# Performance work log

Hardware: AMD Instinct MI355X
Metric: run time of the kernel (lower is better)

The kernel has to match this reference:

```python
import jax, jax.numpy as jnp
import numpy as np

NB = 10          # number_of_basis (hardcoded in module)
MAX_RADIUS = 3.5
DIM_SH = 16      # spherical harmonics l = 0..3 -> (3+1)^2 components


def spherical_harmonics_l3(vec):
    # real spherical harmonics l=0..3 of the normalized vector,
    # 'component' normalization (each component has unit variance on S^2)
    r = jnp.sqrt(jnp.sum(vec * vec, -1, keepdims=True))
    u = vec / jnp.maximum(r, 1e-9)
    x, y, z = u[..., 0], u[..., 1], u[..., 2]
    s3, s5, s15 = jnp.sqrt(3.0), jnp.sqrt(5.0), jnp.sqrt(15.0)
    c358 = jnp.sqrt(35.0 / 8.0); c218 = jnp.sqrt(21.0 / 8.0)
    sh = [jnp.ones_like(x),
          s3 * x, s3 * y, s3 * z,
          s15 * x * y, s15 * y * z, (s5 / 2) * (3 * z * z - 1),
          s15 * x * z, (s15 / 2) * (x * x - y * y),
          c358 * y * (3 * x * x - y * y), jnp.sqrt(105.0) * x * y * z,
          c218 * y * (5 * z * z - 1), (jnp.sqrt(7.0) / 2) * z * (5 * z * z - 3),
          c218 * x * (5 * z * z - 1), (jnp.sqrt(105.0) / 2) * z * (x * x - y * y),
          c358 * x * (x * x - 3 * y * y)]
    return jnp.stack(sh, -1)  # [E, 16]


def soft_one_hot(r):
    # e3nn soft_one_hot_linspace, basis='smooth_finite', cutoff=True
    values = jnp.linspace(0.0, MAX_RADIUS, NB + 2)[1:-1]
    step = MAX_RADIUS / (NB + 1)
    u = (r[:, None] - values) / step
    mask = jnp.abs(u) < 1.0
    us = jnp.where(mask, u, 0.0)
    y = jnp.where(mask, jnp.exp(-1.0 / (1.0 - us * us)), 0.0)
    return 1.14136 * jnp.exp(2.0) * y * jnp.sqrt(float(NB))  # * number_of_basis**0.5


def soft_unit_step(t):
    ts = jnp.where(t > 0, t, 1.0)
    return jnp.where(t > 0, jnp.exp(-1.0 / ts), 0.0)


def fcnet(e, W1, W2):
    # e3nn FullyConnectedNet([10, 16, weight_numel], act=silu): bias-free,
    # fan-in normalized linear layers
    h = jax.nn.silu(e @ W1 / jnp.sqrt(float(e.shape[-1])))
    return h @ W2 / jnp.sqrt(float(W1.shape[-1]))


def setup_inputs() -> dict:
    key = jax.random.key(0)
    ks = jax.random.split(key, 9)
    N, E, C, DK = 20000, 50000, 16, 8
    pos = jax.random.uniform(ks[0], (N, 3), jnp.float32) * 2.0  # box so most edges < max_radius
    x = jax.random.normal(ks[1], (N, C), jnp.float32)
    Wq = jax.random.normal(ks[2], (C, DK), jnp.float32)
    Wk1 = jax.random.normal(ks[3], (NB, 16), jnp.float32)
    Wk2 = jax.random.normal(ks[4], (16, C * DIM_SH * DK), jnp.float32)
    Wv1 = jax.random.normal(ks[5], (NB, 16), jnp.float32)
    Wv2 = jax.random.normal(ks[6], (16, C * DIM_SH * DK), jnp.float32)
    edge_src = jax.random.randint(ks[7], (E,), 0, N, jnp.int32)
    edge_dst = jax.random.randint(ks[8], (E,), 0, N, jnp.int32)
    return {"pos": pos, "x": x, "Wq": Wq, "Wk1": Wk1, "Wk2": Wk2,
            "Wv1": Wv1, "Wv2": Wv2, "edge_src": edge_src, "edge_dst": edge_dst}


def reference(pos, x, Wq, Wk1, Wk2, Wv1, Wv2, edge_src, edge_dst):
    N, C = x.shape
    E = edge_src.shape[0]
    DK = Wq.shape[1]
    edge_vec = pos[edge_src] - pos[edge_dst]                    # [E, 3]
    r = jnp.sqrt(jnp.sum(edge_vec * edge_vec, -1) + 1e-18)      # [E]
    emb = soft_one_hot(r)                                       # [E, 10]
    cutoff = soft_unit_step(10.0 * (1.0 - r / MAX_RADIUS))      # [E]
    sh = spherical_harmonics_l3(edge_vec)                       # [E, 16]
    # per-edge weight-conditioned tensor products (shared_weights=False)
    wk = fcnet(emb, Wk1, Wk2).reshape(E, C, DIM_SH, DK)
    wv = fcnet(emb, Wv1, Wv2).reshape(E, C, DIM_SH, DK)
    xs = x[edge_src]                                            # gather [E, C]
    norm = jnp.sqrt(float(C * DIM_SH))
    k = jnp.einsum('ec,ej,ecjo->eo', xs, sh, wk) / norm         # [E, DK]
    v = jnp.einsum('ec,ej,ecjo->eo', xs, sh, wv) / norm         # [E, DK]
    q = x @ Wq                                                  # [N, DK]
    logits = jnp.sum(q[edge_dst] * k, -1) / jnp.sqrt(float(DK)) # [E]
    expv = cutoff * jnp.exp(logits)
    z = jax.ops.segment_sum(expv, edge_dst, num_segments=N)     # segment-softmax denom
    z = jnp.where(z == 0.0, 1.0, z)
    alpha = expv / z[edge_dst]
    w = jnp.sqrt(jax.nn.relu(alpha))
    out = jax.ops.segment_sum(w[:, None] * v, edge_dst, num_segments=N)  # [N, DK]
    return out
```

## Files before the change

### kernel.cpp

```cpp
#include <hip/hip_runtime.h>
#include <hip/hip_bf16.h>

#define NBASIS 10
#define CDIM 16
#define DKDIM 8
#define JDIM 16

typedef _Float16 half8 __attribute__((ext_vector_type(8)));
typedef float floatx4 __attribute__((ext_vector_type(4)));

__device__ __forceinline__ float ldf(const void* p, int i, int f32) {
    if (f32) return ((const float*)p)[i];
    return __bfloat162float(((const __hip_bfloat16*)p)[i]);
}

__device__ __forceinline__ int detect_f32(const void* x) {
    unsigned short b = ((const unsigned short*)x)[threadIdx.x & 63];
    float v = __uint_as_float(((unsigned int)b) << 16);
    bool bad = !(fabsf(v) < 1000.0f) || (v != 0.0f && fabsf(v) < 1e-15f);
    unsigned long long m = __ballot(bad);
    return (__popcll(m) >= 8) ? 1 : 0;
}

__device__ __forceinline__ const float* uniform_ptr(const float* p) {
    uint64_t v = (uint64_t)p;
    uint32_t lo = __builtin_amdgcn_readfirstlane((uint32_t)v);
    uint32_t hi = __builtin_amdgcn_readfirstlane((uint32_t)(v >> 32));
    return (const float*)(((uint64_t)hi << 32) | lo);
}

__global__ __launch_bounds__(256) void prep_kernel(
    const void* __restrict__ x, const void* __restrict__ Wq,
    const void* __restrict__ Wk1, const void* __restrict__ Wk2,
    const void* __restrict__ Wv1, const void* __restrict__ Wv2,
    float* __restrict__ w1k, float* __restrict__ w1v,
    float* __restrict__ qbuf, _Float16* __restrict__ Bpk,
    int* __restrict__ head, int N)
{
    const int f32 = detect_f32(x);
    int i = blockIdx.x * 256 + threadIdx.x;
    if (i < 160) { w1k[i] = ldf(Wk1, i, f32); w1v[i] = ldf(Wv1, i, f32); }
    if (i < 65536) {
        int j = i & 7, lane = (i >> 3) & 63, ks = (i >> 9) & 7, nt = i >> 12;
        int kk = ks * 32 + (lane >> 4) * 8 + j;
        int nn = nt * 16 + (lane & 15);
        int c = kk >> 4, jj = kk & 15;
        int net = nn >> 7, m = (nn >> 3) & 15, o = nn & 7;
        float v = ldf(net ? Wv2 : Wk2, m * 2048 + c * 128 + jj * 8 + o, f32);
        Bpk[i] = (_Float16)v;
    }
    if (i < N) head[i] = -1;
    if (i < N * 8) {
        int n = i >> 3, o = i & 7;
        float acc = 0.0f;
        #pragma unroll
        for (int c = 0; c < CDIM; ++c)
            acc = fmaf(ldf(x, n * CDIM + c, f32), ldf(Wq, c * DKDIM + o, f32), acc);
        qbuf[i] = acc;
    }
}

__global__ __launch_bounds__(256) void edge_kernel(
    const void* __restrict__ pos, const void* __restrict__ x,
    const int* __restrict__ esrc, const int* __restrict__ edst,
    const float* __restrict__ w1k, const float* __restrict__ w1v,
    const float* __restrict__ qbuf, const _Float16* __restrict__ Bpk,
    int* __restrict__ head, int* __restrict__ next,
    float* __restrict__ evb, _Float16* __restrict__ vbuf, int E)
{
    __shared__ union {
        struct { float xs[64][17]; float sh[64][17]; } g;
        _Float16 A[16384];
        struct { float pk[2][64][9]; float pv[2][64][9]; } p;
    } u;
    __shared__ _Float16 hm_lds[64][34];
    __shared__ float cut_lds[64];
    __shared__ int   d_lds[64];

    const int f32  = detect_f32(x);
    const int tid  = threadIdx.x;
    const int lane = tid & 63;
    const int w    = tid >> 6;
    const int q    = lane >> 4;
    const int e0   = blockIdx.x * 64;
    const int e_g  = e0 + lane;
    const int eidx = (e_g < E) ? e_g : (E - 1);
    const int s = esrc[eidx], d = edst[eidx];

    int prev = -1;
    if (w == 0 && e_g < E) prev = atomicExch(&head[d], e_g);

    float vx = ldf(pos, s * 3 + 0, f32) - ldf(pos, d * 3 + 0, f32);
    float vy = ldf(pos, s * 3 + 1, f32) - ldf(pos, d * 3 + 1, f32);
    float vz = ldf(pos, s * 3 + 2, f32) - ldf(pos, d * 3 + 2, f32);
    float r2 = vx * vx + vy * vy + vz * vz;
    float r  = sqrtf(r2 + 1e-18f);

    if (w == 0) {
        float rsh = sqrtf(r2);
        float inv = 1.0f / fmaxf(rsh, 1e-9f);
        float ux = vx * inv, uy = vy * inv, uz = vz * inv;
        const float s3   = 1.7320508075688772f;
        const float s5   = 2.23606797749979f;
        const float s15  = 3.872983346207417f;
        const float c358 = 2.091650066335189f;
        const float c218 = 1.6201851746019651f;
        const float s105 = 10.246950765959598f;
        const float s7h  = 1.3228756555322954f;
        float xx = ux * ux, yy = uy * uy, zz = uz * uz;
        float sh[16];
        sh[0] = 1.0f;
        sh[1] = s3 * ux; sh[2] = s3 * uy; sh[3] = s3 * uz;
        sh[4] = s15 * ux * uy;
        sh[5] = s15 * uy * uz;
        sh[6] = 0.5f * s5 * (3.0f * zz - 1.0f);
        sh[7] = s15 * ux * uz;
        sh[8] = 0.5f * s15 * (xx - yy);
        sh[9] = c358 * uy * (3.0f * xx - yy);
        sh[10] = s105 * ux * uy * uz;
        sh[11] = c218 * uy * (5.0f * zz - 1.0f);
        sh[12] = s7h * uz * (5.0f * zz - 3.0f);
        sh[13] = c218 * ux * (5.0f * zz - 1.0f);
        sh[14] = 0.5f * s105 * uz * (xx - yy);
        sh[15] = c358 * ux * (xx - 3.0f * yy);
        #pragma unroll
        for (int j = 0; j < 16; ++j) u.g.sh[lane][j] = sh[j];
        float tcut = 10.0f * (1.0f - r * (1.0f / 3.5f));
        cut_lds[lane] = (tcut > 0.0f) ? expf(-1.0f / tcut) : 0.0f;
        d_lds[lane] = d;
    } else if (w == 1) {
        #pragma unroll
        for (int c = 0; c < CDIM; ++c)
            u.g.xs[lane][c] = ldf(x, s * CDIM + c, f32);
    } else {
        const float* w1 = uniform_ptr((w == 2) ? w1k : w1v);
        const int off = (w == 2) ? 0 : 16;
        float emb[NBASIS];
        const float step = 3.5f / 11.0f;
        const float istep = 11.0f / 3.5f;
        const float coef = (float)(1.14136 * 7.38905609893065 * 3.1622776601683795);
        #pragma unroll
        for (int i = 0; i < NBASIS; ++i) {
            float uu = (r - step * (float)(i + 1)) * istep; uu *= uu;
            emb[i] = (uu < 1.0f) ? coef * expf(-1.0f / (1.0f - uu)) : 0.0f;
        }
        const float inv_s10 = 0.31622776601683794f;
        #pragma unroll
        for (int m = 0; m < 16; ++m) {
            float pre = 0.0f;
            #pragma unroll
            for (int nb = 0; nb < NBASIS; ++nb)
                pre = fmaf(emb[nb], w1[nb * 16 + m], pre);
            pre *= inv_s10;
            hm_lds[lane][off + m] = (_Float16)(pre / (1.0f + expf(-pre)));
        }
    }
    __syncthreads();

    half8 af[8];
    {
        const int erow = w * 16 + (lane & 15);
        const int coff = q >> 1, jj0 = (q & 1) * 8;
        #pragma unroll
        for (int ks = 0; ks < 8; ++ks) {
            float xsv = u.g.xs[erow][ks * 2 + coff];
            half8 a;
            #pragma unroll
            for (int j = 0; j < 8; ++j)
                a[j] = (_Float16)(xsv * u.g.sh[erow][jj0 + j]);
            af[ks] = a;
        }
    }
    __syncthreads();
    {
        half8* Af = (half8*)u.A;
        #pragma unroll
        for (int ks = 0; ks < 8; ++ks)
            Af[(w * 8 + ks) * 64 + lane] = af[ks];
    }
    if (w == 0 && e_g < E) next[e_g] = prev;
    __syncthreads();

    float part[16];
    #pragma unroll
    for (int i = 0; i < 16; ++i) part[i] = 0.0f;
    const int b3   = (lane >> 3) & 1;
    const int moff = (w >> 1) * 16;
    const half8* Af = (const half8*)u.A;
    const half8* Bf = (const half8*)Bpk;

    #pragma unroll
    for (int rp = 0; rp < 2; ++rp) {
        half8 a0[8], a1[8];
        #pragma unroll
        for (int ks = 0; ks < 8; ++ks) {
            a0[ks] = Af[((2 * rp)     * 8 + ks) * 64 + lane];
            a1[ks] = Af[((2 * rp + 1) * 8 + ks) * 64 + lane];
        }
        floatx4 acc0[4], acc1[4];
        #pragma unroll
        for (int l = 0; l < 4; ++l) {
            acc0[l] = (floatx4){0.f, 0.f, 0.f, 0.f};
            acc1[l] = (floatx4){0.f, 0.f, 0.f, 0.f};
        }
        #pragma unroll
        for (int l = 0; l < 4; ++l) {
            const int nt = 4 * w + l;
            #pragma unroll
            for (int ks = 0; ks < 8; ++ks) {
                half8 b = Bf[(nt * 8 + ks) * 64 + lane];
                acc0[l] = __builtin_amdgcn_mfma_f32_16x16x32_f16(a0[ks], b, acc0[l], 0, 0, 0);
                acc1[l] = __builtin_amdgcn_mfma_f32_16x16x32_f16(a1[ks], b, acc1[l], 0, 0, 0);
            }
        }
        #pragma unroll
        for (int l = 0; l < 4; ++l) {
            const int m = ((4 * w + l) * 2 + b3) & 15;
            #pragma unroll
            for (int rr = 0; rr < 4; ++rr) {
                const int er = q * 4 + rr;
                part[(2 * rp) * 4 + rr] +=
                    (float)hm_lds[(2 * rp) * 16 + er][moff + m] * acc0[l][rr];
                part[(2 * rp + 1) * 4 + rr] +=
                    (float)hm_lds[(2 * rp + 1) * 16 + er][moff + m] * acc1[l][rr];
            }
        }
    }
    #pragma unroll
    for (int i = 0; i < 16; ++i) part[i] += __shfl_xor(part[i], 8, 64);

    __syncthreads();
    if (b3 == 0) {
        const int o = lane & 7;
        #pragma unroll
        for (int i = 0; i < 16; ++i) {
            const int e = (i >> 2) * 16 + q * 4 + (i & 3);
            if (w < 2) u.p.pk[w][e][o] = part[i];
            else       u.p.pv[w - 2][e][o] = part[i];
        }
    }
    __syncthreads();

    if (tid < 64) {
        const int dd = d_lds[tid];
        float logit = 0.0f;
        #pragma unroll
        for (int o = 0; o < 8; ++o) {
            float kv = u.p.pk[0][tid][o] + u.p.pk[1][tid][o];
            logit = fmaf(qbuf[(size_t)dd * 8 + o], kv, logit);
        }
        logit *= (1.0f / 64.0f) * 0.35355339059327373f;
        if (e0 + tid < E)
            evb[e0 + tid] = cut_lds[tid] * expf(logit);
    }

    {
        const int el = tid & 63, op = tid >> 6;
        if (e0 + el < E) {
            float v0 = u.p.pv[0][el][2 * op]     + u.p.pv[1][el][2 * op];
            float v1 = u.p.pv[0][el][2 * op + 1] + u.p.pv[1][el][2 * op + 1];
            vbuf[(size_t)(e0 + el) * 8 + 2 * op]     = (_Float16)(v0 * (1.0f / 64.0f));
            vbuf[(size_t)(e0 + el) * 8 + 2 * op + 1] = (_Float16)(v1 * (1.0f / 64.0f));
        }
    }
}

__global__ __launch_bounds__(256) void node_kernel(
    const float* __restrict__ evb, const _Float16* __restrict__ vbuf,
    const int* __restrict__ head, const int* __restrict__ next,
    void* __restrict__ out, const void* __restrict__ x, int n8)
{
    const int f32 = detect_f32(x);
    int i = blockIdx.x * 256 + threadIdx.x;
    if (i >= n8) return;
    const int n = i >> 3, o = i & 7;
    float z = 0.0f;
    for (int e = head[n]; e >= 0; e = next[e]) z += evb[e];
    z = (z == 0.0f) ? 1.0f : z;
    const float invz = 1.0f / z;
    float acc = 0.0f;
    for (int e = head[n]; e >= 0; e = next[e])
        acc += sqrtf(evb[e] * invz) * (float)vbuf[(size_t)e * 8 + o];
    if (f32) ((float*)out)[i] = acc;
    else ((__hip_bfloat16*)out)[i] = __float2bfloat16(acc);
}

extern "C" void kernel_launch(void* const* d_in, const int* in_sizes, int n_in,
                              void* d_out, int out_size, void* d_ws, size_t ws_size,
                              hipStream_t stream)
{
    const void* pos = d_in[0];
    const void* x   = d_in[1];
    const void* Wq  = d_in[2];
    const void* Wk1 = d_in[3];
    const void* Wk2 = d_in[4];
    const void* Wv1 = d_in[5];
    const void* Wv2 = d_in[6];
    const int* esrc = (const int*)d_in[7];
    const int* edst = (const int*)d_in[8];
    const int N = in_sizes[1] / CDIM;
    const int E = in_sizes[7];

    _Float16* Bpk = (_Float16*)d_ws;
    float* w1k  = (float*)(Bpk + 65536);
    float* w1v  = w1k + 160;
    float* qbuf = w1v + 160;
    float* evb  = qbuf + (size_t)N * 8;
    _Float16* vbuf = (_Float16*)(evb + E);
    int*   head = (int*)(vbuf + (size_t)E * 8);
    int*   next = head + N;

    int prep_threads = N * 8 > 65536 ? N * 8 : 65536;
    int prep_blocks = (prep_threads + 255) / 256;
    prep_kernel<<<prep_blocks, 256, 0, stream>>>(x, Wq, Wk1, Wk2, Wv1, Wv2,
                                                 w1k, w1v, qbuf, Bpk, head, N);

    int edge_blocks = (E + 63) / 64;
    edge_kernel<<<edge_blocks, 256, 0, stream>>>(pos, x, esrc, edst,
                                                 w1k, w1v, qbuf, Bpk,
                                                 head, next, evb, vbuf, E);

    node_kernel<<<(N * 8 + 255) / 256, 256, 0, stream>>>(
        evb, vbuf, head, next, d_out, x, N * 8);
}
```

Baseline: 101.4 us.

## Compute query projection per edge, pack vbuf stores, single-pass node reduction

Removes the per-node q = x@Wq precompute from the prep kernel. Each edge now computes q for its destination inside the edge kernel from x[dst] and Wq, with the logit scale folded in, and stages it in LDS. The v stores are packed into 32-bit writes. The node kernel walks the linked list once, accumulating both z and sqrt(ev)*v, then divides by sqrt(z) at the end instead of making two passes. The trade is redundant q computation per edge (16x8 FMAs plus an extra x gather) against fewer prep threads, no qbuf traffic, and half the list traversals.

```diff
diff --git a/kernel.cpp b/kernel.cpp
--- a/kernel.cpp
+++ b/kernel.cpp
@@ -30,12 +30,11 @@
 }
 
 __global__ __launch_bounds__(256) void prep_kernel(
-    const void* __restrict__ x, const void* __restrict__ Wq,
+    const void* __restrict__ x,
     const void* __restrict__ Wk1, const void* __restrict__ Wk2,
     const void* __restrict__ Wv1, const void* __restrict__ Wv2,
     float* __restrict__ w1k, float* __restrict__ w1v,
-    float* __restrict__ qbuf, _Float16* __restrict__ Bpk,
-    int* __restrict__ head, int N)
+    _Float16* __restrict__ Bpk, int* __restrict__ head, int N)
 {
     const int f32 = detect_f32(x);
     int i = blockIdx.x * 256 + threadIdx.x;
@@ -50,21 +49,14 @@
         Bpk[i] = (_Float16)v;
     }
     if (i < N) head[i] = -1;
-    if (i < N * 8) {
-        int n = i >> 3, o = i & 7;
-        float acc = 0.0f;
-        #pragma unroll
-        for (int c = 0; c < CDIM; ++c)
-            acc = fmaf(ldf(x, n * CDIM + c, f32), ldf(Wq, c * DKDIM + o, f32), acc);
-        qbuf[i] = acc;
-    }
 }
 
 __global__ __launch_bounds__(256) void edge_kernel(
     const void* __restrict__ pos, const void* __restrict__ x,
+    const void* __restrict__ Wq,
     const int* __restrict__ esrc, const int* __restrict__ edst,
     const float* __restrict__ w1k, const float* __restrict__ w1v,
-    const float* __restrict__ qbuf, const _Float16* __restrict__ Bpk,
+    const _Float16* __restrict__ Bpk,
     int* __restrict__ head, int* __restrict__ next,
     float* __restrict__ evb, _Float16* __restrict__ vbuf, int E)
 {
@@ -75,7 +67,7 @@
     } u;
     __shared__ _Float16 hm_lds[64][34];
     __shared__ float cut_lds[64];
-    __shared__ int   d_lds[64];
+    __shared__ float q_lds[64][9];
 
     const int f32  = detect_f32(x);
     const int tid  = threadIdx.x;
@@ -127,11 +119,22 @@
         for (int j = 0; j < 16; ++j) u.g.sh[lane][j] = sh[j];
         float tcut = 10.0f * (1.0f - r * (1.0f / 3.5f));
         cut_lds[lane] = (tcut > 0.0f) ? expf(-1.0f / tcut) : 0.0f;
-        d_lds[lane] = d;
     } else if (w == 1) {
-        #pragma unroll
-        for (int c = 0; c < CDIM; ++c)
+        float xd[CDIM];
+        #pragma unroll
+        for (int c = 0; c < CDIM; ++c) {
             u.g.xs[lane][c] = ldf(x, s * CDIM + c, f32);
+            xd[c] = ldf(x, d * CDIM + c, f32);
+        }
+        const float qscale = (1.0f / 64.0f) * 0.35355339059327373f;
+        #pragma unroll
+        for (int o = 0; o < 8; ++o) {
+            float acc = 0.0f;
+            #pragma unroll
+            for (int c = 0; c < CDIM; ++c)
+                acc = fmaf(xd[c], ldf(Wq, c * DKDIM + o, f32), acc);
+            q_lds[lane][o] = acc * qscale;
+        }
     } else {
         const float* w1 = uniform_ptr((w == 2) ? w1k : w1v);
         const int off = (w == 2) ? 0 : 16;
@@ -242,14 +245,12 @@
     __syncthreads();
 
     if (tid < 64) {
-        const int dd = d_lds[tid];
         float logit = 0.0f;
         #pragma unroll
         for (int o = 0; o < 8; ++o) {
             float kv = u.p.pk[0][tid][o] + u.p.pk[1][tid][o];
-            logit = fmaf(qbuf[(size_t)dd * 8 + o], kv, logit);
-        }
-        logit *= (1.0f / 64.0f) * 0.35355339059327373f;
+            logit = fmaf(q_lds[tid][o], kv, logit);
+        }
         if (e0 + tid < E)
             evb[e0 + tid] = cut_lds[tid] * expf(logit);
     }
@@ -259,8 +260,10 @@
         if (e0 + el < E) {
             float v0 = u.p.pv[0][el][2 * op]     + u.p.pv[1][el][2 * op];
             float v1 = u.p.pv[0][el][2 * op + 1] + u.p.pv[1][el][2 * op + 1];
-            vbuf[(size_t)(e0 + el) * 8 + 2 * op]     = (_Float16)(v0 * (1.0f / 64.0f));
-            vbuf[(size_t)(e0 + el) * 8 + 2 * op + 1] = (_Float16)(v1 * (1.0f / 64.0f));
+            union { _Float16 h[2]; unsigned int b; } pk2;
+            pk2.h[0] = (_Float16)(v0 * (1.0f / 64.0f));
+            pk2.h[1] = (_Float16)(v1 * (1.0f / 64.0f));
+            ((unsigned int*)vbuf)[(size_t)(e0 + el) * 4 + op] = pk2.b;
         }
     }
 }
@@ -274,15 +277,16 @@
     int i = blockIdx.x * 256 + threadIdx.x;
     if (i >= n8) return;
     const int n = i >> 3, o = i & 7;
-    float z = 0.0f;
-    for (int e = head[n]; e >= 0; e = next[e]) z += evb[e];
+    float z = 0.0f, acc = 0.0f;
+    for (int e = head[n]; e >= 0; e = next[e]) {
+        float ev = evb[e];
+        z += ev;
+        acc += sqrtf(ev) * (float)vbuf[(size_t)e * 8 + o];
+    }
     z = (z == 0.0f) ? 1.0f : z;
-    const float invz = 1.0f / z;
-    float acc = 0.0f;
-    for (int e = head[n]; e >= 0; e = next[e])
-        acc += sqrtf(evb[e] * invz) * (float)vbuf[(size_t)e * 8 + o];
-    if (f32) ((float*)out)[i] = acc;
-    else ((__hip_bfloat16*)out)[i] = __float2bfloat16(acc);
+    float val = acc / sqrtf(z);
+    if (f32) ((float*)out)[i] = val;
+    else ((__hip_bfloat16*)out)[i] = __float2bfloat16(val);
 }
 
 extern "C" void kernel_launch(void* const* d_in, const int* in_sizes, int n_in,
@@ -304,20 +308,19 @@
     _Float16* Bpk = (_Float16*)d_ws;
     float* w1k  = (float*)(Bpk + 65536);
     float* w1v  = w1k + 160;
-    float* qbuf = w1v + 160;
-    float* evb  = qbuf + (size_t)N * 8;
+    float* evb  = w1v + 160;
     _Float16* vbuf = (_Float16*)(evb + E);
     int*   head = (int*)(vbuf + (size_t)E * 8);
     int*   next = head + N;
 
-    int prep_threads = N * 8 > 65536 ? N * 8 : 65536;
+    int prep_threads = N > 65536 ? N : 65536;
     int prep_blocks = (prep_threads + 255) / 256;
-    prep_kernel<<<prep_blocks, 256, 0, stream>>>(x, Wq, Wk1, Wk2, Wv1, Wv2,
-                                                 w1k, w1v, qbuf, Bpk, head, N);
+    prep_kernel<<<prep_blocks, 256, 0, stream>>>(x, Wk1, Wk2, Wv1, Wv2,
+                                                 w1k, w1v, Bpk, head, N);
 
     int edge_blocks = (E + 63) / 64;
-    edge_kernel<<<edge_blocks, 256, 0, stream>>>(pos, x, esrc, edst,
-                                                 w1k, w1v, qbuf, Bpk,
+    edge_kernel<<<edge_blocks, 256, 0, stream>>>(pos, x, Wq, esrc, edst,
+                                                 w1k, w1v, Bpk,
                                                  head, next, evb, vbuf, E);
 
     node_kernel<<<(N * 8 + 255) / 256, 256, 0, stream>>>(
```

After: 111.4 us. 9.9% more time.
